# Performance work log

Hardware: AMD Instinct MI355X
Metric: run time of the kernel (lower is better)

The kernel has to match this reference:

```python
import jax, jax.numpy as jnp
import numpy as np

COMMITMENT_COST = 0.25


def setup_inputs() -> dict:
    key = jax.random.key(0)
    k1, k2 = jax.random.split(key)
    inputs = jax.random.normal(k1, (4, 128, 32, 32, 32), dtype=jnp.float32)
    emb_weight = jax.random.normal(k2, (1024, 128), dtype=jnp.float32)
    return {"inputs": inputs, "emb_weight": emb_weight}


def reference(inputs, emb_weight):
    # inputs: [B, C, D, H, W] with C == embedding_dim; emb_weight: [K, C]
    B, C, D, H, W = inputs.shape
    K = emb_weight.shape[0]

    # flatten to channel-last [N, C]
    flat = jnp.transpose(inputs, (0, 2, 3, 4, 1)).reshape(-1, C)

    x_sq = jnp.sum(flat * flat, axis=1, keepdims=True)            # [N, 1]
    e_sq = jnp.sum(emb_weight * emb_weight, axis=1)[None, :]      # [1, K]
    distances = x_sq + e_sq - 2.0 * (flat @ emb_weight.T)

    # torch.max(-d, dim=1)[1] == argmin(d) (first-occurrence tie-break)
    encoding_indices = jnp.argmin(distances, axis=1)              # [N]
    encoding_indices = encoding_indices.reshape(B, D, H, W)

    # embed + back to channel-first [B, C, D, H, W]
    quantized = jnp.transpose(emb_weight[encoding_indices], (0, 4, 1, 2, 3))

    # eval-mode branch of the source forward
    encodings_sum = jnp.zeros((256,), dtype=jnp.float32)

    loss = COMMITMENT_COST * jnp.mean(
        (jax.lax.stop_gradient(quantized) - inputs) ** 2
    )
    # straight-through estimator
    quantized_st = inputs + jax.lax.stop_gradient(quantized - inputs)

    return (quantized_st, loss, encoding_indices, encodings_sum, emb_weight)
```

## Files before the change

### kernel.cpp

```cpp
#include <hip/hip_runtime.h>

#define SPATIAL 32768
#define NB 4
#define CDIM 128
#define KCODES 1024
#define NROWS (NB * SPATIAL)

#define Q_SIZE (NB * CDIM * SPATIAL)
#define LOSS_OFF Q_SIZE
#define IDX_OFF (Q_SIZE + 1)
#define ESUM_OFF (IDX_OFF + NROWS)
#define EMB_OFF (ESUM_OFF + 256)

#define TCODES 32
#define NT (KCODES / TCODES)
#define MARGIN1 0.06f
#define CAP1 12288
#define NCHUNK 8
#define RB_ROWS 16
#define FINF 3.4e38f
#define LSCALE 1048576.0f

typedef _Float16 half8 __attribute__((ext_vector_type(8)));
typedef float f32x4 __attribute__((ext_vector_type(4)));
typedef unsigned long long ull;

static __device__ __forceinline__ void gload16(const uint4* g, uint4* l) {
    __builtin_amdgcn_global_load_lds(
        (const __attribute__((address_space(1))) unsigned int*)g,
        (__attribute__((address_space(3))) unsigned int*)l, 16, 0, 0);
}

static __device__ __forceinline__ unsigned ford(float f) {
    unsigned u = __float_as_uint(f);
    return (u >> 31) ? ~u : (u | 0x80000000u);
}
static __device__ __forceinline__ float finv(unsigned o) {
    unsigned u = (o & 0x80000000u) ? (o & 0x7FFFFFFFu) : ~o;
    return __uint_as_float(u);
}

__global__ __launch_bounds__(256) void prep_kernel(const float* __restrict__ emb,
                                                   uint4* __restrict__ Bpk16,
                                                   float* __restrict__ ecT,
                                                   float* __restrict__ esq,
                                                   float* __restrict__ out,
                                                   ull* __restrict__ loss_acc,
                                                   int* __restrict__ flag_cnt) {
    if (blockIdx.x >= 64) {
        const int k0 = (blockIdx.x - 64) * 16;
        const int l = threadIdx.x & 15;
        const int gi = threadIdx.x >> 4;
#pragma unroll
        for (int i = 0; i < 8; i++) {
            int c = gi * 8 + i;
            ecT[(size_t)c * KCODES + k0 + l] = emb[(size_t)(k0 + l) * CDIM + c];
        }
        return;
    }

    const int task = blockIdx.x * 256 + threadIdx.x;
    const int k = task >> 4, g = task & 15;

    if (blockIdx.x == 0) {
        if (threadIdx.x == 0) { *loss_acc = 0ULL; *flag_cnt = 0; }
        out[ESUM_OFF + threadIdx.x] = 0.f;
    }

    const float4* e4 = reinterpret_cast<const float4*>(emb + (size_t)k * CDIM + g * 8);
    float4 va = e4[0], vb = e4[1];
    float f[8] = {va.x, va.y, va.z, va.w, vb.x, vb.y, vb.z, vb.w};

    unsigned fpk[4];
    float s = 0.f;
#pragma unroll
    for (int p = 0; p < 4; p++) {
        float v0 = f[2 * p], v1 = f[2 * p + 1];
        union { _Float16 h[2]; unsigned u; } pk;
        pk.h[0] = (_Float16)v0; pk.h[1] = (_Float16)v1;
        fpk[p] = pk.u;
        s = fmaf(v0, v0, s); s = fmaf(v1, v1, s);
    }
    Bpk16[(size_t)k * 16 + (g ^ (k & 15))] = make_uint4(fpk[0], fpk[1], fpk[2], fpk[3]);

#pragma unroll
    for (int i = 0; i < 8; i++)
        out[EMB_OFF + (size_t)k * CDIM + g * 8 + i] = f[i];

    s += __shfl_xor(s, 1); s += __shfl_xor(s, 2);
    s += __shfl_xor(s, 4); s += __shfl_xor(s, 8);
    if (g == 0) esq[k] = s;
}

__global__ __launch_bounds__(256, 4) void score_kernel(const float* __restrict__ in,
                                                       const uint4* __restrict__ Bpk,
                                                       const float* __restrict__ esq,
                                                       const float* __restrict__ emb,
                                                       float* __restrict__ out,
                                                       int* __restrict__ flag_list,
                                                       int* __restrict__ flag_cnt,
                                                       ull* __restrict__ key_ws,
                                                       float* __restrict__ xsq_ws,
                                                       ull* __restrict__ loss_acc) {
    __shared__ uint4 BB[3][TCODES * 16];
    __shared__ float b1L[128];
    __shared__ int   i1L[128];
    __shared__ float xsqL[128];
    __shared__ ull   redL[16];

    const int tid = threadIdx.x;
    const int lane = tid & 63;
    const int w = tid >> 6;
    const int l15 = lane & 15;
    const int lg = lane >> 4;
    const int row0 = blockIdx.x * 128;
    const int b = row0 >> 15;
    const int sbase = (row0 & (SPATIAL - 1)) + w * 32;

#define STAGE(tt, bb)                                                     \
    do {                                                                  \
        const uint4* src_ = Bpk + (size_t)(tt) * 512;                     \
        _Pragma("unroll")                                                 \
        for (int i_ = 0; i_ < 2; i_++)                                    \
            gload16(src_ + i_ * 256 + tid, &BB[bb][i_ * 256 + tid]);      \
    } while (0)

    STAGE(0, 0);
    STAGE(1, 1);

    half8 Af[8];
    float xsq[2] = {0.f, 0.f};
    {
        const float* xb = in + (size_t)b * CDIM * SPATIAL;
#pragma unroll
        for (int kk = 0; kk < 4; kk++)
#pragma unroll
            for (int m = 0; m < 2; m++) {
                int srow = sbase + m * 16 + l15;
                union { unsigned u[4]; half8 h; } pk;
#pragma unroll
                for (int p = 0; p < 4; p++) {
                    int c0 = kk * 32 + lg * 8 + 2 * p;
                    float v0 = xb[(size_t)(c0 + 0) * SPATIAL + srow];
                    float v1 = xb[(size_t)(c0 + 1) * SPATIAL + srow];
                    union { _Float16 h[2]; unsigned u; } q;
                    q.h[0] = (_Float16)v0; q.h[1] = (_Float16)v1;
                    pk.u[p] = q.u;
                    xsq[m] = fmaf(v0, v0, xsq[m]);
                    xsq[m] = fmaf(v1, v1, xsq[m]);
                }
                Af[kk * 2 + m] = pk.h;
            }
    }
#pragma unroll
    for (int m = 0; m < 2; m++) {
        xsq[m] += __shfl_xor(xsq[m], 16);
        xsq[m] += __shfl_xor(xsq[m], 32);
    }
    if (lg == 0) {
        xsqL[w * 32 + l15] = xsq[0];
        xsqL[w * 32 + 16 + l15] = xsq[1];
    }

    float b1[8], b2[8];
    int i1[8];
#pragma unroll
    for (int i = 0; i < 8; i++) { b1[i] = FINF; b2[i] = FINF; i1[i] = 0; }

    for (int t = 0; t < NT; t++) {
        if (t == NT - 1) asm volatile("s_waitcnt vmcnt(0)" ::: "memory");
        else             asm volatile("s_waitcnt vmcnt(2)" ::: "memory");
        __builtin_amdgcn_s_barrier();
        if (t + 2 < NT) STAGE(t + 2, (t + 2) % 3);

        const half8* Bs = reinterpret_cast<const half8*>(BB[t % 3]);
        f32x4 acc[2][2];
#pragma unroll
        for (int m = 0; m < 2; m++)
#pragma unroll
            for (int n = 0; n < 2; n++) acc[m][n] = (f32x4){0.f, 0.f, 0.f, 0.f};

#pragma unroll
        for (int kk = 0; kk < 4; kk++) {
            int phys = (kk * 4 + lg) ^ l15;
            half8 bv[2];
#pragma unroll
            for (int n = 0; n < 2; n++) bv[n] = Bs[(n * 16 + l15) * 16 + phys];
#pragma unroll
            for (int m = 0; m < 2; m++)
#pragma unroll
                for (int n = 0; n < 2; n++)
                    acc[m][n] = __builtin_amdgcn_mfma_f32_16x16x32_f16(Af[kk * 2 + m], bv[n], acc[m][n], 0, 0, 0);
        }

#pragma unroll
        for (int n = 0; n < 2; n++) {
            int col = t * TCODES + n * 16 + l15;
            float ev = esq[col];
#pragma unroll
            for (int m = 0; m < 2; m++)
#pragma unroll
                for (int r = 0; r < 4; r++) {
                    float sv = fmaf(-2.f, acc[m][n][r], ev);
                    int slot = m * 4 + r;
                    bool c = sv < b1[slot];
                    b2[slot] = fminf(fmaxf(sv, b1[slot]), b2[slot]);
                    b1[slot] = fminf(sv, b1[slot]);
                    i1[slot] = c ? col : i1[slot];
                }
        }
    }
#undef STAGE

#pragma unroll
    for (int j = 1; j < 16; j <<= 1) {
#pragma unroll
        for (int slot = 0; slot < 8; slot++) {
            float ob1 = __shfl_xor(b1[slot], j);
            float ob2 = __shfl_xor(b2[slot], j);
            int   oi  = __shfl_xor(i1[slot], j);
            bool take = (ob1 < b1[slot]) || (ob1 == b1[slot] && oi < i1[slot]);
            float nb2 = fminf(fmaxf(b1[slot], ob1), fminf(b2[slot], ob2));
            b1[slot] = take ? ob1 : b1[slot];
            i1[slot] = take ? oi : i1[slot];
            b2[slot] = nb2;
        }
    }

    __syncthreads();

    if (l15 == 0) {
        ull lsum = 0;
#pragma unroll
        for (int m = 0; m < 2; m++)
#pragma unroll
            for (int r = 0; r < 4; r++) {
                int slot = m * 4 + r;
                int rl = w * 32 + m * 16 + lg * 4 + r;
                b1L[rl] = b1[slot];
                i1L[rl] = i1[slot];
                float cexp = b1[slot] + xsqL[rl];
                ull ci = (ull)llrintf(cexp * LSCALE);
                if (b2[slot] - b1[slot] < MARGIN1) {
                    int p = atomicAdd(flag_cnt, 1);
                    if (p < CAP1) {
                        flag_list[p] = row0 + rl;
                        key_ws[p] = ~0ULL;
                        xsq_ws[p] = xsqL[rl];
                        ci = 0;
                    }
                }
                lsum += ci;
            }
        redL[w * 4 + lg] = lsum;
    }
    __syncthreads();
    if (tid == 0) {
        ull s = 0;
#pragma unroll
        for (int i = 0; i < 16; i++) s += redL[i];
        atomicAdd(loss_acc, s);
    }

    {
        const int rl = w * 32 + (lane & 31);
        const int row = row0 + rl;
        const int sp = (row0 & (SPATIAL - 1)) + rl;
        const int k = i1L[rl];
        const int chalf = lane >> 5;

        if (chalf == 0) out[IDX_OFF + row] = (float)k;
        const float4* ep = reinterpret_cast<const float4*>(emb + (size_t)k * CDIM + chalf * 64);
        float* qout = out + (size_t)b * CDIM * SPATIAL + (size_t)chalf * 64 * SPATIAL + sp;
#pragma unroll
        for (int i = 0; i < 16; i++) {
            float4 v = ep[i];
            qout[(size_t)(4 * i + 0) * SPATIAL] = v.x;
            qout[(size_t)(4 * i + 1) * SPATIAL] = v.y;
            qout[(size_t)(4 * i + 2) * SPATIAL] = v.z;
            qout[(size_t)(4 * i + 3) * SPATIAL] = v.w;
        }
    }
}

__global__ __launch_bounds__(256) void xgather_kernel(const float* __restrict__ in,
                                                      const int* __restrict__ flag_list,
                                                      const int* __restrict__ flag_cnt,
                                                      float* __restrict__ xrow_ws) {
    int n1 = *flag_cnt; if (n1 > CAP1) n1 = CAP1;
    const int c = threadIdx.x & 127;
    const int fi = blockIdx.x * 2 + (threadIdx.x >> 7);
    if (fi >= n1) return;
    const int row = flag_list[fi];
    const int bb = row >> 15, sp = row & (SPATIAL - 1);
    xrow_ws[(size_t)fi * CDIM + c] = in[((size_t)bb * CDIM + c) * SPATIAL + sp];
}

__global__ __launch_bounds__(256) void refine_scan_kernel(const float* __restrict__ xrow_ws,
                                                          const float* __restrict__ ecT,
                                                          const float* __restrict__ esq,
                                                          const int* __restrict__ flag_cnt,
                                                          ull* __restrict__ key_ws) {
    __shared__ float xL[RB_ROWS][132];

    int n1 = *flag_cnt; if (n1 > CAP1) n1 = CAP1;
    const int rb = blockIdx.x >> 3;
    const int chunk = blockIdx.x & 7;
    const int base = rb * RB_ROWS;
    if (base >= n1) return;

    const int t = threadIdx.x;
    const int row = t >> 4;
    const int l = t & 15;

    {
        const float4* src = reinterpret_cast<const float4*>(xrow_ws + (size_t)(base + row) * CDIM);
        float4* dst = reinterpret_cast<float4*>(&xL[row][0]);
        dst[l * 2] = src[l * 2];
        dst[l * 2 + 1] = src[l * 2 + 1];
    }
    __syncthreads();

    const float4* e4 = reinterpret_cast<const float4*>(ecT);
    const int cbase = chunk * 32 + l;

    f32x4 accA = {0.f, 0.f, 0.f, 0.f};
    f32x4 accB = {0.f, 0.f, 0.f, 0.f};
#pragma unroll 8
    for (int c = 0; c < CDIM; c++) {
        float xx = xL[row][c];
        float4 va = e4[(size_t)c * 256 + cbase];
        float4 vb = e4[(size_t)c * 256 + cbase + 16];
        accA[0] = fmaf(va.x, xx, accA[0]);
        accA[1] = fmaf(va.y, xx, accA[1]);
        accA[2] = fmaf(va.z, xx, accA[2]);
        accA[3] = fmaf(va.w, xx, accA[3]);
        accB[0] = fmaf(vb.x, xx, accB[0]);
        accB[1] = fmaf(vb.y, xx, accB[1]);
        accB[2] = fmaf(vb.z, xx, accB[2]);
        accB[3] = fmaf(vb.w, xx, accB[3]);
    }

    const int kA = chunk * 128 + 4 * l;
    const int kB = kA + 64;
    ull key = ~0ULL;
#pragma unroll
    for (int j = 0; j < 4; j++) {
        float dA = fmaf(-2.f, accA[j], esq[kA + j]);
        ull cA = ((ull)ford(dA) << 32) | (unsigned)(kA + j);
        key = (cA < key) ? cA : key;
        float dB = fmaf(-2.f, accB[j], esq[kB + j]);
        ull cB = ((ull)ford(dB) << 32) | (unsigned)(kB + j);
        key = (cB < key) ? cB : key;
    }

#pragma unroll
    for (int m = 1; m < 16; m <<= 1) {
        ull o = __shfl_xor(key, m);
        key = (o < key) ? o : key;
    }
    if (l == 0 && base + row < n1) atomicMin(&key_ws[base + row], key);
}

__global__ __launch_bounds__(128) void refine_emit_kernel(const float* __restrict__ emb,
                                                          const int* __restrict__ flag_list,
                                                          const int* __restrict__ flag_cnt,
                                                          const ull* __restrict__ key_ws,
                                                          const float* __restrict__ xsq_ws,
                                                          float* __restrict__ out,
                                                          ull* __restrict__ loss_acc) {
    __shared__ int sOld;
    int n1 = *flag_cnt; if (n1 > CAP1) n1 = CAP1;
    const int t = threadIdx.x;

    for (int p = blockIdx.x; p < n1; p += gridDim.x) {
        const ull key = key_ws[p];
        const int idx = (int)(key & 0xFFFFFFFFu);
        const float d = finv((unsigned)(key >> 32));
        const int row = flag_list[p];
        const int bb = row >> 15, sp = row & (SPATIAL - 1);

        if (t == 0) sOld = (int)out[IDX_OFF + row];
        __syncthreads();
        const int oldidx = sOld;

        if (t == 0) {
            atomicAdd(loss_acc, (ull)llrintf((d + xsq_ws[p]) * LSCALE));
            if (idx != oldidx) out[IDX_OFF + row] = (float)idx;
        }
        if (idx != oldidx)
            out[(size_t)bb * CDIM * SPATIAL + (size_t)t * SPATIAL + sp] =
                emb[(size_t)idx * CDIM + t];
        __syncthreads();
    }
}

__global__ void finalize_kernel(const ull* __restrict__ loss_acc,
                                float* __restrict__ out) {
    double s = (double)*loss_acc / (double)LSCALE;
    out[LOSS_OFF] = (float)(0.25 * s / (double)Q_SIZE);
}

extern "C" void kernel_launch(void* const* d_in, const int* in_sizes, int n_in,
                              void* d_out, int out_size, void* d_ws, size_t ws_size,
                              hipStream_t stream) {
    const float* in = (const float*)d_in[0];
    const float* emb = (const float*)d_in[1];
    float* out = (float*)d_out;

    float* esq = (float*)d_ws;
    uint4* Bpk16 = (uint4*)(esq + 4096);
    float* ecT = (float*)(Bpk16 + 16384);
    ull* key_ws = (ull*)(ecT + CDIM * KCODES);
    float* xsq_ws = (float*)(key_ws + CAP1);
    float* xrow_ws = xsq_ws + CAP1;
    ull* loss_acc = (ull*)(xrow_ws + (size_t)CAP1 * CDIM);
    int* flag_cnt = (int*)(loss_acc + 1);
    int* flag_list = flag_cnt + 1;

    prep_kernel<<<128, 256, 0, stream>>>(emb, Bpk16, ecT, esq, out,
                                         loss_acc, flag_cnt);
    score_kernel<<<NROWS / 128, 256, 0, stream>>>(in, Bpk16, esq, emb, out,
                                                  flag_list, flag_cnt,
                                                  key_ws, xsq_ws, loss_acc);
    xgather_kernel<<<CAP1 / 2, 256, 0, stream>>>(in, flag_list, flag_cnt, xrow_ws);
    refine_scan_kernel<<<(CAP1 / RB_ROWS) * NCHUNK, 256, 0, stream>>>(
        xrow_ws, ecT, esq, flag_cnt, key_ws);
    refine_emit_kernel<<<2048, 128, 0, stream>>>(emb, flag_list, flag_cnt,
                                                 key_ws, xsq_ws, out, loss_acc);
    finalize_kernel<<<1, 1, 0, stream>>>(loss_acc, out);
}
```

Baseline: 132.1 us.

## Double rows per score block and fuse flagged-row gather into score kernel

```diff
diff --git a/kernel.cpp b/kernel.cpp
--- a/kernel.cpp
+++ b/kernel.cpp
@@ -92,30 +92,33 @@
     if (g == 0) esq[k] = s;
 }
 
-__global__ __launch_bounds__(256, 4) void score_kernel(const float* __restrict__ in,
-                                                       const uint4* __restrict__ Bpk,
-                                                       const float* __restrict__ esq,
-                                                       const float* __restrict__ emb,
-                                                       float* __restrict__ out,
-                                                       int* __restrict__ flag_list,
-                                                       int* __restrict__ flag_cnt,
-                                                       ull* __restrict__ key_ws,
-                                                       float* __restrict__ xsq_ws,
-                                                       ull* __restrict__ loss_acc) {
+__global__ __launch_bounds__(256) void score_kernel(const float* __restrict__ in,
+                                                    const uint4* __restrict__ Bpk,
+                                                    const float* __restrict__ esq,
+                                                    const float* __restrict__ emb,
+                                                    float* __restrict__ out,
+                                                    int* __restrict__ flag_list,
+                                                    int* __restrict__ flag_cnt,
+                                                    ull* __restrict__ key_ws,
+                                                    float* __restrict__ xsq_ws,
+                                                    float* __restrict__ xrow_ws,
+                                                    ull* __restrict__ loss_acc) {
     __shared__ uint4 BB[3][TCODES * 16];
-    __shared__ float b1L[128];
-    __shared__ int   i1L[128];
-    __shared__ float xsqL[128];
+    __shared__ int   i1L[256];
+    __shared__ float xsqL[256];
     __shared__ ull   redL[16];
+    __shared__ int   defRows[256];
+    __shared__ int   defP[256];
+    __shared__ int   defCnt;
 
     const int tid = threadIdx.x;
     const int lane = tid & 63;
     const int w = tid >> 6;
     const int l15 = lane & 15;
     const int lg = lane >> 4;
-    const int row0 = blockIdx.x * 128;
+    const int row0 = blockIdx.x * 256;
     const int b = row0 >> 15;
-    const int sbase = (row0 & (SPATIAL - 1)) + w * 32;
+    const int sbase = (row0 & (SPATIAL - 1)) + w * 64;
 
 #define STAGE(tt, bb)                                                     \
     do {                                                                  \
@@ -128,14 +131,16 @@
     STAGE(0, 0);
     STAGE(1, 1);
 
-    half8 Af[8];
-    float xsq[2] = {0.f, 0.f};
+    if (tid == 0) defCnt = 0;
+
+    half8 Af[16];
+    float xsq[4] = {0.f, 0.f, 0.f, 0.f};
     {
         const float* xb = in + (size_t)b * CDIM * SPATIAL;
 #pragma unroll
         for (int kk = 0; kk < 4; kk++)
 #pragma unroll
-            for (int m = 0; m < 2; m++) {
+            for (int m = 0; m < 4; m++) {
                 int srow = sbase + m * 16 + l15;
                 union { unsigned u[4]; half8 h; } pk;
 #pragma unroll
@@ -149,23 +154,24 @@
                     xsq[m] = fmaf(v0, v0, xsq[m]);
                     xsq[m] = fmaf(v1, v1, xsq[m]);
                 }
-                Af[kk * 2 + m] = pk.h;
+                Af[kk * 4 + m] = pk.h;
             }
     }
 #pragma unroll
-    for (int m = 0; m < 2; m++) {
+    for (int m = 0; m < 4; m++) {
         xsq[m] += __shfl_xor(xsq[m], 16);
         xsq[m] += __shfl_xor(xsq[m], 32);
     }
     if (lg == 0) {
-        xsqL[w * 32 + l15] = xsq[0];
-        xsqL[w * 32 + 16 + l15] = xsq[1];
-    }
-
-    float b1[8], b2[8];
-    int i1[8];
-#pragma unroll
-    for (int i = 0; i < 8; i++) { b1[i] = FINF; b2[i] = FINF; i1[i] = 0; }
+#pragma unroll
+        for (int m = 0; m < 4; m++)
+            xsqL[w * 64 + m * 16 + l15] = xsq[m];
+    }
+
+    float b1[16], b2[16];
+    int i1[16];
+#pragma unroll
+    for (int i = 0; i < 16; i++) { b1[i] = FINF; b2[i] = FINF; i1[i] = 0; }
 
     for (int t = 0; t < NT; t++) {
         if (t == NT - 1) asm volatile("s_waitcnt vmcnt(0)" ::: "memory");
@@ -174,9 +180,9 @@
         if (t + 2 < NT) STAGE(t + 2, (t + 2) % 3);
 
         const half8* Bs = reinterpret_cast<const half8*>(BB[t % 3]);
-        f32x4 acc[2][2];
-#pragma unroll
-        for (int m = 0; m < 2; m++)
+        f32x4 acc[4][2];
+#pragma unroll
+        for (int m = 0; m < 4; m++)
 #pragma unroll
             for (int n = 0; n < 2; n++) acc[m][n] = (f32x4){0.f, 0.f, 0.f, 0.f};
 
@@ -187,10 +193,10 @@
 #pragma unroll
             for (int n = 0; n < 2; n++) bv[n] = Bs[(n * 16 + l15) * 16 + phys];
 #pragma unroll
-            for (int m = 0; m < 2; m++)
+            for (int m = 0; m < 4; m++)
 #pragma unroll
                 for (int n = 0; n < 2; n++)
-                    acc[m][n] = __builtin_amdgcn_mfma_f32_16x16x32_f16(Af[kk * 2 + m], bv[n], acc[m][n], 0, 0, 0);
+                    acc[m][n] = __builtin_amdgcn_mfma_f32_16x16x32_f16(Af[kk * 4 + m], bv[n], acc[m][n], 0, 0, 0);
         }
 
 #pragma unroll
@@ -198,7 +204,7 @@
             int col = t * TCODES + n * 16 + l15;
             float ev = esq[col];
 #pragma unroll
-            for (int m = 0; m < 2; m++)
+            for (int m = 0; m < 4; m++)
 #pragma unroll
                 for (int r = 0; r < 4; r++) {
                     float sv = fmaf(-2.f, acc[m][n][r], ev);
@@ -215,7 +221,7 @@
 #pragma unroll
     for (int j = 1; j < 16; j <<= 1) {
 #pragma unroll
-        for (int slot = 0; slot < 8; slot++) {
+        for (int slot = 0; slot < 16; slot++) {
             float ob1 = __shfl_xor(b1[slot], j);
             float ob2 = __shfl_xor(b2[slot], j);
             int   oi  = __shfl_xor(i1[slot], j);
@@ -232,12 +238,11 @@
     if (l15 == 0) {
         ull lsum = 0;
 #pragma unroll
-        for (int m = 0; m < 2; m++)
+        for (int m = 0; m < 4; m++)
 #pragma unroll
             for (int r = 0; r < 4; r++) {
                 int slot = m * 4 + r;
-                int rl = w * 32 + m * 16 + lg * 4 + r;
-                b1L[rl] = b1[slot];
+                int rl = w * 64 + m * 16 + lg * 4 + r;
                 i1L[rl] = i1[slot];
                 float cexp = b1[slot] + xsqL[rl];
                 ull ci = (ull)llrintf(cexp * LSCALE);
@@ -248,6 +253,9 @@
                         key_ws[p] = ~0ULL;
                         xsq_ws[p] = xsqL[rl];
                         ci = 0;
+                        int d = atomicAdd(&defCnt, 1);
+                        defRows[d] = rl;
+                        defP[d] = p;
                     }
                 }
                 lsum += ci;
@@ -263,17 +271,15 @@
     }
 
     {
-        const int rl = w * 32 + (lane & 31);
+        const int rl = tid;
         const int row = row0 + rl;
         const int sp = (row0 & (SPATIAL - 1)) + rl;
         const int k = i1L[rl];
-        const int chalf = lane >> 5;
-
-        if (chalf == 0) out[IDX_OFF + row] = (float)k;
-        const float4* ep = reinterpret_cast<const float4*>(emb + (size_t)k * CDIM + chalf * 64);
-        float* qout = out + (size_t)b * CDIM * SPATIAL + (size_t)chalf * 64 * SPATIAL + sp;
-#pragma unroll
-        for (int i = 0; i < 16; i++) {
+        out[IDX_OFF + row] = (float)k;
+        const float4* ep = reinterpret_cast<const float4*>(emb + (size_t)k * CDIM);
+        float* qout = out + (size_t)b * CDIM * SPATIAL + sp;
+#pragma unroll
+        for (int i = 0; i < 32; i++) {
             float4 v = ep[i];
             qout[(size_t)(4 * i + 0) * SPATIAL] = v.x;
             qout[(size_t)(4 * i + 1) * SPATIAL] = v.y;
@@ -281,19 +287,18 @@
             qout[(size_t)(4 * i + 3) * SPATIAL] = v.w;
         }
     }
-}
-
-__global__ __launch_bounds__(256) void xgather_kernel(const float* __restrict__ in,
-                                                      const int* __restrict__ flag_list,
-                                                      const int* __restrict__ flag_cnt,
-                                                      float* __restrict__ xrow_ws) {
-    int n1 = *flag_cnt; if (n1 > CAP1) n1 = CAP1;
-    const int c = threadIdx.x & 127;
-    const int fi = blockIdx.x * 2 + (threadIdx.x >> 7);
-    if (fi >= n1) return;
-    const int row = flag_list[fi];
-    const int bb = row >> 15, sp = row & (SPATIAL - 1);
-    xrow_ws[(size_t)fi * CDIM + c] = in[((size_t)bb * CDIM + c) * SPATIAL + sp];
+
+    {
+        const int nd = defCnt;
+        const int c = tid & 127;
+        for (int di = tid >> 7; di < nd; di += 2) {
+            const int rl = defRows[di];
+            const int p = defP[di];
+            const int sp = (row0 & (SPATIAL - 1)) + rl;
+            xrow_ws[(size_t)p * CDIM + c] =
+                in[((size_t)b * CDIM + c) * SPATIAL + sp];
+        }
+    }
 }
 
 __global__ __launch_bounds__(256) void refine_scan_kernel(const float* __restrict__ xrow_ws,
@@ -420,10 +425,9 @@
 
     prep_kernel<<<128, 256, 0, stream>>>(emb, Bpk16, ecT, esq, out,
                                          loss_acc, flag_cnt);
-    score_kernel<<<NROWS / 128, 256, 0, stream>>>(in, Bpk16, esq, emb, out,
+    score_kernel<<<NROWS / 256, 256, 0, stream>>>(in, Bpk16, esq, emb, out,
                                                   flag_list, flag_cnt,
-                                                  key_ws, xsq_ws, loss_acc);
-    xgather_kernel<<<CAP1 / 2, 256, 0, stream>>>(in, flag_list, flag_cnt, xrow_ws);
+                                                  key_ws, xsq_ws, xrow_ws, loss_acc);
     refine_scan_kernel<<<(CAP1 / RB_ROWS) * NCHUNK, 256, 0, stream>>>(
         xrow_ws, ecT, esq, flag_cnt, key_ws);
     refine_emit_kernel<<<2048, 128, 0, stream>>>(emb, flag_list, flag_cnt,
```

Result: slower. 176.5 us (+33.6%).

## Fuse gather into score kernel and emit into refine scan via completion counter

Applied to the files above, without the earlier changes.

```diff
diff --git a/kernel.cpp b/kernel.cpp
--- a/kernel.cpp
+++ b/kernel.cpp
@@ -101,12 +101,16 @@
                                                        int* __restrict__ flag_cnt,
                                                        ull* __restrict__ key_ws,
                                                        float* __restrict__ xsq_ws,
+                                                       int* __restrict__ done_ws,
+                                                       float* __restrict__ xrow_ws,
                                                        ull* __restrict__ loss_acc) {
     __shared__ uint4 BB[3][TCODES * 16];
-    __shared__ float b1L[128];
     __shared__ int   i1L[128];
     __shared__ float xsqL[128];
     __shared__ ull   redL[16];
+    __shared__ int   defRows[128];
+    __shared__ int   defP[128];
+    __shared__ int   defCnt;
 
     const int tid = threadIdx.x;
     const int lane = tid & 63;
@@ -127,6 +131,8 @@
 
     STAGE(0, 0);
     STAGE(1, 1);
+
+    if (tid == 0) defCnt = 0;
 
     half8 Af[8];
     float xsq[2] = {0.f, 0.f};
@@ -237,7 +243,6 @@
             for (int r = 0; r < 4; r++) {
                 int slot = m * 4 + r;
                 int rl = w * 32 + m * 16 + lg * 4 + r;
-                b1L[rl] = b1[slot];
                 i1L[rl] = i1[slot];
                 float cexp = b1[slot] + xsqL[rl];
                 ull ci = (ull)llrintf(cexp * LSCALE);
@@ -247,7 +252,11 @@
                         flag_list[p] = row0 + rl;
                         key_ws[p] = ~0ULL;
                         xsq_ws[p] = xsqL[rl];
+                        done_ws[p] = 0;
                         ci = 0;
+                        int d = atomicAdd(&defCnt, 1);
+                        defRows[d] = rl;
+                        defP[d] = p;
                     }
                 }
                 lsum += ci;
@@ -281,26 +290,31 @@
             qout[(size_t)(4 * i + 3) * SPATIAL] = v.w;
         }
     }
-}
-
-__global__ __launch_bounds__(256) void xgather_kernel(const float* __restrict__ in,
-                                                      const int* __restrict__ flag_list,
-                                                      const int* __restrict__ flag_cnt,
-                                                      float* __restrict__ xrow_ws) {
-    int n1 = *flag_cnt; if (n1 > CAP1) n1 = CAP1;
-    const int c = threadIdx.x & 127;
-    const int fi = blockIdx.x * 2 + (threadIdx.x >> 7);
-    if (fi >= n1) return;
-    const int row = flag_list[fi];
-    const int bb = row >> 15, sp = row & (SPATIAL - 1);
-    xrow_ws[(size_t)fi * CDIM + c] = in[((size_t)bb * CDIM + c) * SPATIAL + sp];
+
+    {
+        const int nd = defCnt;
+        const int c = tid & 127;
+        for (int di = tid >> 7; di < nd; di += 2) {
+            const int rl = defRows[di];
+            const int p = defP[di];
+            const int sp = (row0 & (SPATIAL - 1)) + rl;
+            xrow_ws[(size_t)p * CDIM + c] =
+                in[((size_t)b * CDIM + c) * SPATIAL + sp];
+        }
+    }
 }
 
 __global__ __launch_bounds__(256) void refine_scan_kernel(const float* __restrict__ xrow_ws,
                                                           const float* __restrict__ ecT,
                                                           const float* __restrict__ esq,
+                                                          const float* __restrict__ emb,
+                                                          const int* __restrict__ flag_list,
                                                           const int* __restrict__ flag_cnt,
-                                                          ull* __restrict__ key_ws) {
+                                                          ull* __restrict__ key_ws,
+                                                          const float* __restrict__ xsq_ws,
+                                                          int* __restrict__ done_ws,
+                                                          float* __restrict__ out,
+                                                          ull* __restrict__ loss_acc) {
     __shared__ float xL[RB_ROWS][132];
 
     int n1 = *flag_cnt; if (n1 > CAP1) n1 = CAP1;
@@ -310,8 +324,11 @@
     if (base >= n1) return;
 
     const int t = threadIdx.x;
+    const int lane = t & 63;
     const int row = t >> 4;
     const int l = t & 15;
+    const int fi = base + row;
+    const bool valid = (fi < n1);
 
     {
         const float4* src = reinterpret_cast<const float4*>(xrow_ws + (size_t)(base + row) * CDIM);
@@ -359,39 +376,40 @@
         ull o = __shfl_xor(key, m);
         key = (o < key) ? o : key;
     }
-    if (l == 0 && base + row < n1) atomicMin(&key_ws[base + row], key);
-}
-
-__global__ __launch_bounds__(128) void refine_emit_kernel(const float* __restrict__ emb,
-                                                          const int* __restrict__ flag_list,
-                                                          const int* __restrict__ flag_cnt,
-                                                          const ull* __restrict__ key_ws,
-                                                          const float* __restrict__ xsq_ws,
-                                                          float* __restrict__ out,
-                                                          ull* __restrict__ loss_acc) {
-    __shared__ int sOld;
-    int n1 = *flag_cnt; if (n1 > CAP1) n1 = CAP1;
-    const int t = threadIdx.x;
-
-    for (int p = blockIdx.x; p < n1; p += gridDim.x) {
-        const ull key = key_ws[p];
-        const int idx = (int)(key & 0xFFFFFFFFu);
-        const float d = finv((unsigned)(key >> 32));
-        const int row = flag_list[p];
-        const int bb = row >> 15, sp = row & (SPATIAL - 1);
-
-        if (t == 0) sOld = (int)out[IDX_OFF + row];
-        __syncthreads();
-        const int oldidx = sOld;
-
-        if (t == 0) {
-            atomicAdd(loss_acc, (ull)llrintf((d + xsq_ws[p]) * LSCALE));
-            if (idx != oldidx) out[IDX_OFF + row] = (float)idx;
-        }
-        if (idx != oldidx)
-            out[(size_t)bb * CDIM * SPATIAL + (size_t)t * SPATIAL + sp] =
-                emb[(size_t)idx * CDIM + t];
-        __syncthreads();
+
+    int trig = 0;
+    if (l == 0 && valid) {
+        atomicMin(&key_ws[fi], key);
+        __threadfence();
+        int old = atomicAdd(&done_ws[fi], 1);
+        trig = (old == NCHUNK - 1);
+    }
+    trig = __shfl(trig, (int)(lane & 48));
+
+    if (trig) {
+        int idx = 0, oldidx = 0;
+        float d = 0.f;
+        const int rowid = flag_list[fi];
+        if (l == 0) {
+            __threadfence();
+            ull kv = *((volatile ull*)&key_ws[fi]);
+            idx = (int)(kv & 0xFFFFFFFFu);
+            d = finv((unsigned)(kv >> 32));
+            oldidx = (int)out[IDX_OFF + rowid];
+            atomicAdd(loss_acc, (ull)llrintf((d + xsq_ws[fi]) * LSCALE));
+            if (idx != oldidx) out[IDX_OFF + rowid] = (float)idx;
+        }
+        idx = __shfl(idx, (int)(lane & 48));
+        oldidx = __shfl(oldidx, (int)(lane & 48));
+        if (idx != oldidx) {
+            const int bb = rowid >> 15, sp = rowid & (SPATIAL - 1);
+#pragma unroll
+            for (int i = 0; i < 8; i++) {
+                int c = l * 8 + i;
+                out[(size_t)bb * CDIM * SPATIAL + (size_t)c * SPATIAL + sp] =
+                    emb[(size_t)idx * CDIM + c];
+            }
+        }
     }
 }
 
@@ -413,7 +431,8 @@
     float* ecT = (float*)(Bpk16 + 16384);
     ull* key_ws = (ull*)(ecT + CDIM * KCODES);
     float* xsq_ws = (float*)(key_ws + CAP1);
-    float* xrow_ws = xsq_ws + CAP1;
+    int* done_ws = (int*)(xsq_ws + CAP1);
+    float* xrow_ws = (float*)(done_ws + CAP1);
     ull* loss_acc = (ull*)(xrow_ws + (size_t)CAP1 * CDIM);
     int* flag_cnt = (int*)(loss_acc + 1);
     int* flag_list = flag_cnt + 1;
@@ -422,11 +441,10 @@
                                          loss_acc, flag_cnt);
     score_kernel<<<NROWS / 128, 256, 0, stream>>>(in, Bpk16, esq, emb, out,
                                                   flag_list, flag_cnt,
-                                                  key_ws, xsq_ws, loss_acc);
-    xgather_kernel<<<CAP1 / 2, 256, 0, stream>>>(in, flag_list, flag_cnt, xrow_ws);
+                                                  key_ws, xsq_ws, done_ws,
+                                                  xrow_ws, loss_acc);
     refine_scan_kernel<<<(CAP1 / RB_ROWS) * NCHUNK, 256, 0, stream>>>(
-        xrow_ws, ecT, esq, flag_cnt, key_ws);
-    refine_emit_kernel<<<2048, 128, 0, stream>>>(emb, flag_list, flag_cnt,
-                                                 key_ws, xsq_ws, out, loss_acc);
+        xrow_ws, ecT, esq, emb, flag_list, flag_cnt,
+        key_ws, xsq_ws, done_ws, out, loss_acc);
     finalize_kernel<<<1, 1, 0, stream>>>(loss_acc, out);
 }
```

Measured after the change: 148.0 us. 1.12x slower.

## Read codebook fragments directly from global memory instead of LDS staging

Applied to the files above, without the earlier changes.

```diff
diff --git a/kernel.cpp b/kernel.cpp
--- a/kernel.cpp
+++ b/kernel.cpp
@@ -24,12 +24,6 @@
 typedef _Float16 half8 __attribute__((ext_vector_type(8)));
 typedef float f32x4 __attribute__((ext_vector_type(4)));
 typedef unsigned long long ull;
-
-static __device__ __forceinline__ void gload16(const uint4* g, uint4* l) {
-    __builtin_amdgcn_global_load_lds(
-        (const __attribute__((address_space(1))) unsigned int*)g,
-        (__attribute__((address_space(3))) unsigned int*)l, 16, 0, 0);
-}
 
 static __device__ __forceinline__ unsigned ford(float f) {
     unsigned u = __float_as_uint(f);
@@ -81,7 +75,8 @@
         fpk[p] = pk.u;
         s = fmaf(v0, v0, s); s = fmaf(v1, v1, s);
     }
-    Bpk16[(size_t)k * 16 + (g ^ (k & 15))] = make_uint4(fpk[0], fpk[1], fpk[2], fpk[3]);
+    Bpk16[(size_t)(k >> 5) * 512 + (size_t)g * 32 + (k & 31)] =
+        make_uint4(fpk[0], fpk[1], fpk[2], fpk[3]);
 
 #pragma unroll
     for (int i = 0; i < 8; i++)
@@ -102,8 +97,6 @@
                                                        ull* __restrict__ key_ws,
                                                        float* __restrict__ xsq_ws,
                                                        ull* __restrict__ loss_acc) {
-    __shared__ uint4 BB[3][TCODES * 16];
-    __shared__ float b1L[128];
     __shared__ int   i1L[128];
     __shared__ float xsqL[128];
     __shared__ ull   redL[16];
@@ -116,17 +109,6 @@
     const int row0 = blockIdx.x * 128;
     const int b = row0 >> 15;
     const int sbase = (row0 & (SPATIAL - 1)) + w * 32;
-
-#define STAGE(tt, bb)                                                     \
-    do {                                                                  \
-        const uint4* src_ = Bpk + (size_t)(tt) * 512;                     \
-        _Pragma("unroll")                                                 \
-        for (int i_ = 0; i_ < 2; i_++)                                    \
-            gload16(src_ + i_ * 256 + tid, &BB[bb][i_ * 256 + tid]);      \
-    } while (0)
-
-    STAGE(0, 0);
-    STAGE(1, 1);
 
     half8 Af[8];
     float xsq[2] = {0.f, 0.f};
@@ -167,13 +149,9 @@
 #pragma unroll
     for (int i = 0; i < 8; i++) { b1[i] = FINF; b2[i] = FINF; i1[i] = 0; }
 
+    const half8* Bg = reinterpret_cast<const half8*>(Bpk);
     for (int t = 0; t < NT; t++) {
-        if (t == NT - 1) asm volatile("s_waitcnt vmcnt(0)" ::: "memory");
-        else             asm volatile("s_waitcnt vmcnt(2)" ::: "memory");
-        __builtin_amdgcn_s_barrier();
-        if (t + 2 < NT) STAGE(t + 2, (t + 2) % 3);
-
-        const half8* Bs = reinterpret_cast<const half8*>(BB[t % 3]);
+        const half8* Bs = Bg + (size_t)t * 512;
         f32x4 acc[2][2];
 #pragma unroll
         for (int m = 0; m < 2; m++)
@@ -182,10 +160,10 @@
 
 #pragma unroll
         for (int kk = 0; kk < 4; kk++) {
-            int phys = (kk * 4 + lg) ^ l15;
             half8 bv[2];
 #pragma unroll
-            for (int n = 0; n < 2; n++) bv[n] = Bs[(n * 16 + l15) * 16 + phys];
+            for (int n = 0; n < 2; n++)
+                bv[n] = Bs[(kk * 4 + lg) * 32 + n * 16 + l15];
 #pragma unroll
             for (int m = 0; m < 2; m++)
 #pragma unroll
@@ -210,7 +188,6 @@
                 }
         }
     }
-#undef STAGE
 
 #pragma unroll
     for (int j = 1; j < 16; j <<= 1) {
@@ -237,7 +214,6 @@
             for (int r = 0; r < 4; r++) {
                 int slot = m * 4 + r;
                 int rl = w * 32 + m * 16 + lg * 4 + r;
-                b1L[rl] = b1[slot];
                 i1L[rl] = i1[slot];
                 float cexp = b1[slot] + xsqL[rl];
                 ull ci = (ull)llrintf(cexp * LSCALE);
```

After: 134.7 us. No clear change (+2.0%).
